# Performance work log

Measured on AMD Instinct MI355X. Metric: run time of the kernel, lower is better.

Reference implementation:

```python
import jax, jax.numpy as jnp
import numpy as np

LATENT, HID, STYLE, D, B = 16, 512, 64, 8, 16384


def _lin(key, fan_in, fan_out):
    kw, kb = jax.random.split(key)
    s = 1.0 / np.sqrt(fan_in)
    return (jax.random.uniform(kw, (fan_in, fan_out), jnp.float32, -s, s),
            jax.random.uniform(kb, (fan_out,), jnp.float32, -s, s))


def setup_inputs() -> dict:
    key = jax.random.key(0)
    ks = jax.random.split(key, 12)
    x = jax.random.normal(ks[0], (B, LATENT), jnp.float32)
    y = jax.random.randint(ks[1], (B,), 0, D)
    # shared MLP: latent->512, 512->512 x3, each followed by ReLU
    W0, b0 = _lin(ks[2], LATENT, HID)
    W1, b1 = _lin(ks[3], HID, HID)
    W2, b2 = _lin(ks[4], HID, HID)
    W3, b3 = _lin(ks[5], HID, HID)
    # unshared per-domain 4-layer MLPs, stacked along domain axis d
    def _stack(k, fi, fo):
        Ws, bs = [], []
        for kk in jax.random.split(k, D):
            w, b = _lin(kk, fi, fo)
            Ws.append(w); bs.append(b)
        return jnp.stack(Ws), jnp.stack(bs)
    U0, c0 = _stack(ks[6], HID, HID)
    U1, c1 = _stack(ks[7], HID, HID)
    U2, c2 = _stack(ks[8], HID, HID)
    U3, c3 = _stack(ks[9], HID, STYLE)
    return {"x": x, "y": y,
            "W0": W0, "b0": b0, "W1": W1, "b1": b1,
            "W2": W2, "b2": b2, "W3": W3, "b3": b3,
            "U0": U0, "c0": c0, "U1": U1, "c1": c1,
            "U2": U2, "c2": c2, "U3": U3, "c3": c3}


def reference(x, y, W0, b0, W1, b1, W2, b2, W3, b3,
              U0, c0, U1, c1, U2, c2, U3, c3):
    # shared trunk
    h = jax.nn.relu(x @ W0 + b0)
    h = jax.nn.relu(h @ W1 + b1)
    h = jax.nn.relu(h @ W2 + b2)
    h = jax.nn.relu(h @ W3 + b3)            # [B, HID]
    # run all D expert MLPs batched, then select per-sample by domain y
    g = jax.nn.relu(jnp.einsum('bi,dio->dbo', h, U0) + c0[:, None, :])
    g = jax.nn.relu(jnp.einsum('dbi,dio->dbo', g, U1) + c1[:, None, :])
    g = jax.nn.relu(jnp.einsum('dbi,dio->dbo', g, U2) + c2[:, None, :])
    g = jnp.einsum('dbi,dio->dbo', g, U3) + c3[:, None, :]   # [D, B, STYLE]
    out = g[y, jnp.arange(g.shape[1])]       # [B, STYLE]
    return out
```

## Files before the change

### kernel.cpp

```cpp
#include <hip/hip_runtime.h>

typedef _Float16 f16;
typedef _Float16 f16x4 __attribute__((ext_vector_type(4)));
typedef _Float16 f16x8 __attribute__((ext_vector_type(8)));
typedef float f32x4 __attribute__((ext_vector_type(4)));

#define B_TOT 16384
#define HID_  512
#define LAT_  16
#define STY_  64
#define ND_   8

#define ROWS 64
#define NTHR 512
#define NBLK 256

__global__ void prep_k(const float* W0, f16* Wt0, const float* W1, f16* Wt1,
                       const float* W2, f16* Wt2, const float* W3, f16* Wt3,
                       const float* U0, f16* U0t, const float* U1, f16* U1t,
                       const float* U2, f16* U2t, const float* U3, f16* U3t) {
  int z = blockIdx.z;
  const float* src; f16* dst; int Kin, Nin, Kpad, NR;
  if (z == 0)      { src = W0; dst = Wt0; Kin = 16;  Nin = 512; Kpad = 32;  NR = 512; }
  else if (z == 1) { src = W1; dst = Wt1; Kin = 512; Nin = 512; Kpad = 512; NR = 512; }
  else if (z == 2) { src = W2; dst = Wt2; Kin = 512; Nin = 512; Kpad = 512; NR = 512; }
  else if (z == 3) { src = W3; dst = Wt3; Kin = 512; Nin = 512; Kpad = 512; NR = 512; }
  else if (z < 12) { int d = z - 4;  src = U0 + (long)d * 262144; dst = U0t + (long)d * 262144; Kin = 512; Nin = 512; Kpad = 512; NR = 512; }
  else if (z < 20) { int d = z - 12; src = U1 + (long)d * 262144; dst = U1t + (long)d * 262144; Kin = 512; Nin = 512; Kpad = 512; NR = 512; }
  else if (z < 28) { int d = z - 20; src = U2 + (long)d * 262144; dst = U2t + (long)d * 262144; Kin = 512; Nin = 512; Kpad = 512; NR = 512; }
  else             { int d = z - 28; src = U3 + (long)d * 32768;  dst = U3t + (long)d * 32768;  Kin = 512; Nin = 64;  Kpad = 512; NR = 64; }

  __shared__ float tile[32][33];
  int k0 = blockIdx.y * 32, n0 = blockIdx.x * 32;
  int tx = threadIdx.x, ty = threadIdx.y;
  #pragma unroll
  for (int i = 0; i < 32; i += 8) {
    int k = k0 + ty + i, n = n0 + tx;
    tile[ty + i][tx] = (k < Kin && n < Nin) ? src[(long)k * Nin + n] : 0.f;
  }
  __syncthreads();
  #pragma unroll
  for (int i = 0; i < 32; i += 8) {
    int n = n0 + ty + i, k = k0 + tx;
    if (n < NR && k < Kpad)
      dst[(long)(((k >> 5) * NR + n) << 5) | (k & 31)] = (f16)tile[tx][ty + i];
  }
}

#define NT_BUCKET 1024
#define RPT 16

__global__ __launch_bounds__(NT_BUCKET) void bucket_k(const int* __restrict__ y,
                                                      int* __restrict__ offsets,
                                                      int* __restrict__ perm) {
  __shared__ int hist[ND_][NT_BUCKET];
  __shared__ int totals[ND_];
  __shared__ int bases[ND_ + 1];
  int t = threadIdx.x;
  int base = t * RPT;

  #pragma unroll
  for (int d = 0; d < ND_; d++) hist[d][t] = 0;
  int yv[RPT];
  #pragma unroll
  for (int i = 0; i < RPT; i++) {
    yv[i] = y[base + i];
    hist[yv[i]][t]++;
  }
  __syncthreads();

  int wave = t >> 6, lane = t & 63;
  if (wave < ND_) {
    int d = wave;
    int carry = 0;
    for (int c = 0; c < NT_BUCKET; c += 64) {
      int v = hist[d][c + lane];
      int s = v;
      #pragma unroll
      for (int off = 1; off < 64; off <<= 1) {
        int u = __shfl_up(s, off, 64);
        if (lane >= off) s += u;
      }
      hist[d][c + lane] = carry + s - v;
      carry += __shfl(s, 63, 64);
    }
    if (lane == 0) totals[d] = carry;
  }
  __syncthreads();

  if (t == 0) {
    int s = 0;
    #pragma unroll
    for (int d = 0; d < ND_; d++) { bases[d] = s; offsets[d] = s; s += totals[d]; }
    bases[ND_] = s; offsets[ND_] = s;
  }
  __syncthreads();

  #pragma unroll
  for (int i = 0; i < RPT; i++) {
    int d = yv[i];
    int pos = bases[d] + hist[d][t];
    hist[d][t]++;
    perm[pos] = base + i;
  }
}

template<int KT, bool FINAL>
__device__ __forceinline__ void do_layer(
    const f16* __restrict__ Wk, const float* __restrict__ bias,
    f16* __restrict__ act, int rlo, int rhi,
    const int* __restrict__ perm, int slot0, float* __restrict__ out, int t) {
  const int lane = t & 63, wid = t >> 6;
  const int lr = lane & 15, lg = lane >> 4;
  char* actb = (char*)act;

  __syncthreads();

  if (!FINAL) {
    const int wn = wid * 64;
    const f16* wp[4];
    #pragma unroll
    for (int n = 0; n < 4; n++)
      wp[n] = Wk + ((wn + n * 16 + lr) * 32 + lg * 8);

    f32x4 acc[4][4];
    #pragma unroll
    for (int m = 0; m < 4; m++)
      #pragma unroll
      for (int n = 0; n < 4; n++) acc[m][n] = f32x4{0.f, 0.f, 0.f, 0.f};

    f16x8 ba[4], bb[4];
    #pragma unroll
    for (int n = 0; n < 4; n++) ba[n] = *(const f16x8*)(wp[n]);

    #define STEP_(kt, BC, BN_, PF) do {                                       \
      if (PF) {                                                               \
        _Pragma("unroll")                                                     \
        for (int n = 0; n < 4; n++)                                           \
          BN_[n] = *(const f16x8*)(wp[n] + ((kt) + 1) * 16384);               \
      }                                                                       \
      f16x8 af[4];                                                            \
      _Pragma("unroll")                                                       \
      for (int m = 0; m < 4; m++) {                                           \
        int r = m * 16 + lr;                                                  \
        af[m] = *(const f16x8*)(actb + r * 1024 +                             \
                ((((kt) * 32 + lg * 8) * 2) ^ ((r & 7) << 4)));               \
      }                                                                       \
      _Pragma("unroll")                                                       \
      for (int m = 0; m < 4; m++)                                             \
        _Pragma("unroll")                                                     \
        for (int n = 0; n < 4; n++)                                           \
          acc[m][n] = __builtin_amdgcn_mfma_f32_16x16x32_f16(BC[n], af[m], acc[m][n], 0, 0, 0); \
    } while (0)

    if constexpr (KT == 1) {
      STEP_(0, ba, bb, false);
    } else {
      #pragma unroll 2
      for (int kt2 = 0; kt2 < KT - 2; kt2 += 2) {
        STEP_(kt2, ba, bb, true);
        STEP_(kt2 + 1, bb, ba, true);
      }
      STEP_(KT - 2, ba, bb, true);
      STEP_(KT - 1, bb, ba, false);
    }
    #undef STEP_

    __syncthreads();

    #pragma unroll
    for (int m = 0; m < 4; m++) {
      int r = m * 16 + lr;
      bool ok = (r >= rlo) && (r < rhi);
      #pragma unroll
      for (int n = 0; n < 4; n++) {
        int cn0 = wn + n * 16 + lg * 4;
        f32x4 bb2 = *(const f32x4*)(bias + cn0);
        f16x4 h;
        #pragma unroll
        for (int j = 0; j < 4; j++)
          h[j] = (f16)fmaxf(acc[m][n][j] + bb2[j], 0.f);
        if (ok)
          *(f16x4*)(actb + r * 1024 + ((cn0 * 2) ^ ((r & 7) << 4))) = h;
      }
    }
  } else {
    const int m0 = (wid >> 2) * 32;
    const int wn = (wid & 3) * 16;
    const f16* wp0 = Wk + ((wn + lr) * 32 + lg * 8);
    f32x4 a0 = f32x4{0.f, 0.f, 0.f, 0.f}, a1 = a0;
    #pragma unroll 4
    for (int kt = 0; kt < 16; kt++) {
      f16x8 bf = *(const f16x8*)(wp0 + kt * 2048);
      int r0 = m0 + lr, r1 = m0 + 16 + lr;
      f16x8 af0 = *(const f16x8*)(actb + r0 * 1024 +
                   (((kt * 32 + lg * 8) * 2) ^ ((r0 & 7) << 4)));
      f16x8 af1 = *(const f16x8*)(actb + r1 * 1024 +
                   (((kt * 32 + lg * 8) * 2) ^ ((r1 & 7) << 4)));
      a0 = __builtin_amdgcn_mfma_f32_16x16x32_f16(bf, af0, a0, 0, 0, 0);
      a1 = __builtin_amdgcn_mfma_f32_16x16x32_f16(bf, af1, a1, 0, 0, 0);
    }
    int cn0 = wn + lg * 4;
    f32x4 bb2 = *(const f32x4*)(bias + cn0);
    #pragma unroll
    for (int m = 0; m < 2; m++) {
      int r = m0 + m * 16 + lr;
      if (r >= rlo && r < rhi) {
        int orig = perm[slot0 + r];
        f32x4 v;
        #pragma unroll
        for (int j = 0; j < 4; j++) v[j] = (m ? a1[j] : a0[j]) + bb2[j];
        *(f32x4*)(out + (long)orig * STY_ + cn0) = v;
      }
    }
  }
}

__global__ __launch_bounds__(NTHR, 2) void fused_k(
    const float* __restrict__ x,
    const f16* __restrict__ Wt0, const float* __restrict__ b0,
    const f16* __restrict__ Wt1, const float* __restrict__ b1,
    const f16* __restrict__ Wt2, const float* __restrict__ b2,
    const f16* __restrict__ Wt3, const float* __restrict__ b3,
    const f16* __restrict__ U0t, const float* __restrict__ c0,
    const f16* __restrict__ U1t, const float* __restrict__ c1,
    const f16* __restrict__ U2t, const float* __restrict__ c2,
    const f16* __restrict__ U3t, const float* __restrict__ c3,
    const int* __restrict__ offs, const int* __restrict__ perm,
    float* __restrict__ out) {
  __shared__ f16 act[ROWS * 512];

  int t = threadIdx.x;
  int wg = (blockIdx.x & 7) * (NBLK / 8) + (blockIdx.x >> 3);
  int slot0 = wg * ROWS;

  char* actb = (char*)act;
  #pragma unroll
  for (int i = 0; i < 4; i++) {
    int e = i * NTHR + t;
    int r = e >> 5, c = e & 31;
    int orig = perm[slot0 + r];
    f16 v = (c < LAT_) ? (f16)x[orig * LAT_ + c] : (f16)0.f;
    *(f16*)(actb + r * 1024 + ((c * 2) ^ ((r & 7) << 4))) = v;
  }

  int d0 = 0, d1 = 0;
  #pragma unroll
  for (int d = 1; d < ND_; d++) {
    d0 += (slot0 >= offs[d]);
    d1 += (slot0 + ROWS - 1 >= offs[d]);
  }

  do_layer<1,  false>(Wt0, b0, act, 0, ROWS, perm, slot0, out, t);
  do_layer<16, false>(Wt1, b1, act, 0, ROWS, perm, slot0, out, t);
  do_layer<16, false>(Wt2, b2, act, 0, ROWS, perm, slot0, out, t);
  do_layer<16, false>(Wt3, b3, act, 0, ROWS, perm, slot0, out, t);

  #pragma unroll 1
  for (int d = d0; d <= d1; d++) {
    int rlo = (d == d0) ? 0 : (offs[d] - slot0);
    int rhi = (d == d1) ? ROWS : (offs[d + 1] - slot0);
    do_layer<16, false>(U0t + (long)d * 262144, c0 + d * 512,
                        act, rlo, rhi, perm, slot0, out, t);
  }
  #pragma unroll 1
  for (int d = d0; d <= d1; d++) {
    int rlo = (d == d0) ? 0 : (offs[d] - slot0);
    int rhi = (d == d1) ? ROWS : (offs[d + 1] - slot0);
    do_layer<16, false>(U1t + (long)d * 262144, c1 + d * 512,
                        act, rlo, rhi, perm, slot0, out, t);
  }
  #pragma unroll 1
  for (int d = d0; d <= d1; d++) {
    int rlo = (d == d0) ? 0 : (offs[d] - slot0);
    int rhi = (d == d1) ? ROWS : (offs[d + 1] - slot0);
    do_layer<16, false>(U2t + (long)d * 262144, c2 + d * 512,
                        act, rlo, rhi, perm, slot0, out, t);
  }
  #pragma unroll 1
  for (int d = d0; d <= d1; d++) {
    int rlo = (d == d0) ? 0 : (offs[d] - slot0);
    int rhi = (d == d1) ? ROWS : (offs[d + 1] - slot0);
    do_layer<16, true>(U3t + (long)d * 32768, c3 + d * 64,
                       act, rlo, rhi, perm, slot0, out, t);
  }
}


extern "C" void kernel_launch(void* const* d_in, const int* in_sizes, int n_in,
                              void* d_out, int out_size, void* d_ws, size_t ws_size,
                              hipStream_t stream) {
  const float* x  = (const float*)d_in[0];
  const int*   y  = (const int*)  d_in[1];
  const float* W0 = (const float*)d_in[2];
  const float* b0 = (const float*)d_in[3];
  const float* W1 = (const float*)d_in[4];
  const float* b1 = (const float*)d_in[5];
  const float* W2 = (const float*)d_in[6];
  const float* b2 = (const float*)d_in[7];
  const float* W3 = (const float*)d_in[8];
  const float* b3 = (const float*)d_in[9];
  const float* U0 = (const float*)d_in[10];
  const float* c0 = (const float*)d_in[11];
  const float* U1 = (const float*)d_in[12];
  const float* c1 = (const float*)d_in[13];
  const float* U2 = (const float*)d_in[14];
  const float* c2 = (const float*)d_in[15];
  const float* U3 = (const float*)d_in[16];
  const float* c3 = (const float*)d_in[17];
  float* out = (float*)d_out;

  char* p = (char*)d_ws;
  auto alloc = [&](size_t bytes) -> char* {
    char* r = p; p += (bytes + 255) & ~(size_t)255; return r;
  };
  f16* Wt0 = (f16*)alloc((size_t)512 * 32 * 2);
  f16* Wt1 = (f16*)alloc((size_t)512 * 512 * 2);
  f16* Wt2 = (f16*)alloc((size_t)512 * 512 * 2);
  f16* Wt3 = (f16*)alloc((size_t)512 * 512 * 2);
  f16* U0t = (f16*)alloc((size_t)ND_ * 512 * 512 * 2);
  f16* U1t = (f16*)alloc((size_t)ND_ * 512 * 512 * 2);
  f16* U2t = (f16*)alloc((size_t)ND_ * 512 * 512 * 2);
  f16* U3t = (f16*)alloc((size_t)ND_ * 16 * 64 * 32 * 2);
  int* offsets = (int*)alloc((ND_ + 1) * 4);
  int* perm    = (int*)alloc((size_t)B_TOT * 4);

  prep_k<<<dim3(16, 16, 36), dim3(32, 8), 0, stream>>>(W0, Wt0, W1, Wt1, W2, Wt2, W3, Wt3,
                                                       U0, U0t, U1, U1t, U2, U2t, U3, U3t);
  bucket_k<<<1, NT_BUCKET, 0, stream>>>(y, offsets, perm);
  fused_k<<<NBLK, NTHR, 0, stream>>>(x, Wt0, b0, Wt1, b1, Wt2, b2, Wt3, b3,
                                     U0t, c0, U1t, c1, U2t, c2, U3t, c3,
                                     offsets, perm, out);
}
```

Baseline: 120.0 us.

## Double threads per block, shrink per-wave tiles, and use k-blocked LDS layout

Raises the block size from 512 to 1024 threads (16 waves), so each wave computes a 64x32 output tile instead of 64x64. This halves the accumulator registers and raises the launch-bounds occupancy target. The activation buffer in LDS moves from a row-major XOR-swizzled layout to a k-chunk-blocked layout (32 columns by 64 rows per chunk), which makes fragment addressing simple and linear. The final layer gives each of the 16 waves one 16x16 tile, and the K loop is fully unrolled with explicit A/B double buffering. The trade-off is that each wave now reuses every weight fragment across less work, and the unswizzled layout may add LDS bank conflicts.

```diff
diff --git a/kernel.cpp b/kernel.cpp
--- a/kernel.cpp
+++ b/kernel.cpp
@@ -6,13 +6,12 @@
 typedef float f32x4 __attribute__((ext_vector_type(4)));
 
 #define B_TOT 16384
-#define HID_  512
 #define LAT_  16
 #define STY_  64
 #define ND_   8
 
 #define ROWS 64
-#define NTHR 512
+#define NTHR 1024
 #define NBLK 256
 
 __global__ void prep_k(const float* W0, f16* Wt0, const float* W1, f16* Wt1,
@@ -105,6 +104,8 @@
   }
 }
 
+#define MFMA_(b, a, c) __builtin_amdgcn_mfma_f32_16x16x32_f16((b), (a), (c), 0, 0, 0)
+
 template<int KT, bool FINAL>
 __device__ __forceinline__ void do_layer(
     const f16* __restrict__ Wk, const float* __restrict__ bias,
@@ -117,54 +118,59 @@
   __syncthreads();
 
   if (!FINAL) {
-    const int wn = wid * 64;
-    const f16* wp[4];
-    #pragma unroll
-    for (int n = 0; n < 4; n++)
-      wp[n] = Wk + ((wn + n * 16 + lr) * 32 + lg * 8);
-
-    f32x4 acc[4][4];
+    const int wn = wid * 32;
+    const f16* wp0 = Wk + ((wn + lr) * 32 + lg * 8);
+    const f16* wp1 = Wk + ((wn + 16 + lr) * 32 + lg * 8);
+    const char* ab[4];
     #pragma unroll
     for (int m = 0; m < 4; m++)
-      #pragma unroll
-      for (int n = 0; n < 4; n++) acc[m][n] = f32x4{0.f, 0.f, 0.f, 0.f};
-
-    f16x8 ba[4], bb[4];
-    #pragma unroll
-    for (int n = 0; n < 4; n++) ba[n] = *(const f16x8*)(wp[n]);
-
-    #define STEP_(kt, BC, BN_, PF) do {                                       \
-      if (PF) {                                                               \
-        _Pragma("unroll")                                                     \
-        for (int n = 0; n < 4; n++)                                           \
-          BN_[n] = *(const f16x8*)(wp[n] + ((kt) + 1) * 16384);               \
-      }                                                                       \
-      f16x8 af[4];                                                            \
-      _Pragma("unroll")                                                       \
-      for (int m = 0; m < 4; m++) {                                           \
-        int r = m * 16 + lr;                                                  \
-        af[m] = *(const f16x8*)(actb + r * 1024 +                             \
-                ((((kt) * 32 + lg * 8) * 2) ^ ((r & 7) << 4)));               \
-      }                                                                       \
-      _Pragma("unroll")                                                       \
-      for (int m = 0; m < 4; m++)                                             \
-        _Pragma("unroll")                                                     \
-        for (int n = 0; n < 4; n++)                                           \
-          acc[m][n] = __builtin_amdgcn_mfma_f32_16x16x32_f16(BC[n], af[m], acc[m][n], 0, 0, 0); \
-    } while (0)
+      ab[m] = actb + (m * 16 + lr) * 64 + lg * 16;
+
+    f32x4 acc[4][2];
+    #pragma unroll
+    for (int m = 0; m < 4; m++) {
+      acc[m][0] = f32x4{0.f, 0.f, 0.f, 0.f};
+      acc[m][1] = f32x4{0.f, 0.f, 0.f, 0.f};
+    }
+
+    f16x8 a0[4], a1[4], b00, b01, b10, b11;
+    b00 = *(const f16x8*)wp0;
+    b01 = *(const f16x8*)wp1;
+    #pragma unroll
+    for (int m = 0; m < 4; m++) a0[m] = *(const f16x8*)(ab[m]);
 
     if constexpr (KT == 1) {
-      STEP_(0, ba, bb, false);
+      #pragma unroll
+      for (int m = 0; m < 4; m++) {
+        acc[m][0] = MFMA_(b00, a0[m], acc[m][0]);
+        acc[m][1] = MFMA_(b01, a0[m], acc[m][1]);
+      }
     } else {
-      #pragma unroll 2
-      for (int kt2 = 0; kt2 < KT - 2; kt2 += 2) {
-        STEP_(kt2, ba, bb, true);
-        STEP_(kt2 + 1, bb, ba, true);
+      #pragma unroll
+      for (int kt2 = 0; kt2 < KT / 2; kt2++) {
+        const int k1 = 2 * kt2 + 1, k2 = 2 * kt2 + 2;
+        b10 = *(const f16x8*)(wp0 + k1 * 16384);
+        b11 = *(const f16x8*)(wp1 + k1 * 16384);
+        #pragma unroll
+        for (int m = 0; m < 4; m++) a1[m] = *(const f16x8*)(ab[m] + k1 * 4096);
+        #pragma unroll
+        for (int m = 0; m < 4; m++) {
+          acc[m][0] = MFMA_(b00, a0[m], acc[m][0]);
+          acc[m][1] = MFMA_(b01, a0[m], acc[m][1]);
+        }
+        if (kt2 < KT / 2 - 1) {
+          b00 = *(const f16x8*)(wp0 + k2 * 16384);
+          b01 = *(const f16x8*)(wp1 + k2 * 16384);
+          #pragma unroll
+          for (int m = 0; m < 4; m++) a0[m] = *(const f16x8*)(ab[m] + k2 * 4096);
+        }
+        #pragma unroll
+        for (int m = 0; m < 4; m++) {
+          acc[m][0] = MFMA_(b10, a1[m], acc[m][0]);
+          acc[m][1] = MFMA_(b11, a1[m], acc[m][1]);
+        }
       }
-      STEP_(KT - 2, ba, bb, true);
-      STEP_(KT - 1, bb, ba, false);
-    }
-    #undef STEP_
+    }
 
     __syncthreads();
 
@@ -173,50 +179,42 @@
       int r = m * 16 + lr;
       bool ok = (r >= rlo) && (r < rhi);
       #pragma unroll
-      for (int n = 0; n < 4; n++) {
-        int cn0 = wn + n * 16 + lg * 4;
-        f32x4 bb2 = *(const f32x4*)(bias + cn0);
+      for (int n = 0; n < 2; n++) {
+        int cl = n * 16 + lg * 4;
+        f32x4 bb = *(const f32x4*)(bias + wn + cl);
         f16x4 h;
         #pragma unroll
         for (int j = 0; j < 4; j++)
-          h[j] = (f16)fmaxf(acc[m][n][j] + bb2[j], 0.f);
+          h[j] = (f16)fmaxf(acc[m][n][j] + bb[j], 0.f);
         if (ok)
-          *(f16x4*)(actb + r * 1024 + ((cn0 * 2) ^ ((r & 7) << 4))) = h;
+          *(f16x4*)(actb + wid * 4096 + r * 64 + cl * 2) = h;
       }
     }
   } else {
-    const int m0 = (wid >> 2) * 32;
-    const int wn = (wid & 3) * 16;
-    const f16* wp0 = Wk + ((wn + lr) * 32 + lg * 8);
-    f32x4 a0 = f32x4{0.f, 0.f, 0.f, 0.f}, a1 = a0;
-    #pragma unroll 4
+    const int mf = wid >> 2, nf = wid & 3;
+    const f16* wp = Wk + ((nf * 16 + lr) * 32 + lg * 8);
+    const char* abf = actb + (mf * 16 + lr) * 64 + lg * 16;
+    f32x4 a = f32x4{0.f, 0.f, 0.f, 0.f};
+    #pragma unroll
     for (int kt = 0; kt < 16; kt++) {
-      f16x8 bf = *(const f16x8*)(wp0 + kt * 2048);
-      int r0 = m0 + lr, r1 = m0 + 16 + lr;
-      f16x8 af0 = *(const f16x8*)(actb + r0 * 1024 +
-                   (((kt * 32 + lg * 8) * 2) ^ ((r0 & 7) << 4)));
-      f16x8 af1 = *(const f16x8*)(actb + r1 * 1024 +
-                   (((kt * 32 + lg * 8) * 2) ^ ((r1 & 7) << 4)));
-      a0 = __builtin_amdgcn_mfma_f32_16x16x32_f16(bf, af0, a0, 0, 0, 0);
-      a1 = __builtin_amdgcn_mfma_f32_16x16x32_f16(bf, af1, a1, 0, 0, 0);
-    }
-    int cn0 = wn + lg * 4;
-    f32x4 bb2 = *(const f32x4*)(bias + cn0);
-    #pragma unroll
-    for (int m = 0; m < 2; m++) {
-      int r = m0 + m * 16 + lr;
-      if (r >= rlo && r < rhi) {
-        int orig = perm[slot0 + r];
-        f32x4 v;
-        #pragma unroll
-        for (int j = 0; j < 4; j++) v[j] = (m ? a1[j] : a0[j]) + bb2[j];
-        *(f32x4*)(out + (long)orig * STY_ + cn0) = v;
-      }
-    }
-  }
-}
-
-__global__ __launch_bounds__(NTHR, 2) void fused_k(
+      f16x8 bf = *(const f16x8*)(wp + kt * 2048);
+      f16x8 af = *(const f16x8*)(abf + kt * 4096);
+      a = MFMA_(bf, af, a);
+    }
+    int r = mf * 16 + lr;
+    if (r >= rlo && r < rhi) {
+      int orig = perm[slot0 + r];
+      int cn0 = nf * 16 + lg * 4;
+      f32x4 bb = *(const f32x4*)(bias + cn0);
+      f32x4 v;
+      #pragma unroll
+      for (int j = 0; j < 4; j++) v[j] = a[j] + bb[j];
+      *(f32x4*)(out + (long)orig * STY_ + cn0) = v;
+    }
+  }
+}
+
+__global__ __launch_bounds__(NTHR, 4) void fused_k(
     const float* __restrict__ x,
     const f16* __restrict__ Wt0, const float* __restrict__ b0,
     const f16* __restrict__ Wt1, const float* __restrict__ b1,
@@ -228,7 +226,7 @@
     const f16* __restrict__ U3t, const float* __restrict__ c3,
     const int* __restrict__ offs, const int* __restrict__ perm,
     float* __restrict__ out) {
-  __shared__ f16 act[ROWS * 512];
+  __shared__ f16 act[16 * 64 * 32];
 
   int t = threadIdx.x;
   int wg = (blockIdx.x & 7) * (NBLK / 8) + (blockIdx.x >> 3);
@@ -236,12 +234,12 @@
 
   char* actb = (char*)act;
   #pragma unroll
-  for (int i = 0; i < 4; i++) {
+  for (int i = 0; i < 2; i++) {
     int e = i * NTHR + t;
     int r = e >> 5, c = e & 31;
     int orig = perm[slot0 + r];
     f16 v = (c < LAT_) ? (f16)x[orig * LAT_ + c] : (f16)0.f;
-    *(f16*)(actb + r * 1024 + ((c * 2) ^ ((r & 7) << 4))) = v;
+    *(f16*)(actb + r * 64 + c * 2) = v;
   }
 
   int d0 = 0, d1 = 0;
```

New measurement: 120.7 us. About the same (+0.6%).
